# Kernel optimization log

Hardware: AMD Instinct MI355X
Metric: run time of the kernel (lower is better)

## Reference

```python
import jax, jax.numpy as jnp
import numpy as np

INPUT_SIZE = 128
HIDDEN_SIZE = 128
B, S = 4, 4096


def setup_inputs() -> dict:
    key = jax.random.key(0)
    ks = jax.random.split(key, 9)
    sc_in = 1.0 / np.sqrt(INPUT_SIZE)
    sc_h = 1.0 / np.sqrt(HIDDEN_SIZE)
    return {
        "x": jax.random.normal(ks[0], (B, S, INPUT_SIZE), jnp.float32),
        "Wq": jax.random.uniform(ks[1], (INPUT_SIZE, HIDDEN_SIZE), jnp.float32, -sc_in, sc_in),
        "bq": jax.random.uniform(ks[2], (HIDDEN_SIZE,), jnp.float32, -sc_in, sc_in),
        "Wk": jax.random.uniform(ks[3], (INPUT_SIZE, HIDDEN_SIZE), jnp.float32, -sc_in, sc_in),
        "bk": jax.random.uniform(ks[4], (HIDDEN_SIZE,), jnp.float32, -sc_in, sc_in),
        "Wv": jax.random.uniform(ks[5], (INPUT_SIZE, HIDDEN_SIZE), jnp.float32, -sc_in, sc_in),
        "bv": jax.random.uniform(ks[6], (HIDDEN_SIZE,), jnp.float32, -sc_in, sc_in),
        "Wo": jax.random.uniform(ks[7], (HIDDEN_SIZE, INPUT_SIZE), jnp.float32, -sc_h, sc_h),
        "bo": jax.random.uniform(ks[8], (INPUT_SIZE,), jnp.float32, -sc_h, sc_h),
    }


def reference(x, Wq, bq, Wk, bk, Wv, bv, Wo, bo):
    # single-head scaled dot-product attention (non-causal), dropout is eval-mode identity
    q = x @ Wq + bq                      # [B, S, H]
    k = x @ Wk + bk                      # [B, S, H]
    v = x @ Wv + bv                      # [B, S, H]
    scale = 1.0 / jnp.sqrt(jnp.asarray(HIDDEN_SIZE, x.dtype))
    scores = jnp.einsum("bsh,bth->bst", q, k) * scale   # [B, S, S]
    attn = jax.nn.softmax(scores, axis=-1)
    attended = jnp.einsum("bst,bth->bsh", attn, v)       # [B, S, H]
    return attended @ Wo + bo                            # [B, S, input_size]
```

## Files before the change

### kernel.cpp

```cpp
#include <hip/hip_runtime.h>
#include <stdint.h>

typedef __attribute__((ext_vector_type(8))) short short8;
typedef __attribute__((ext_vector_type(4))) float f32x4;
typedef __attribute__((ext_vector_type(16))) float f32x16;
typedef __attribute__((ext_vector_type(4))) int i32x4;
typedef __attribute__((ext_vector_type(2))) int i32x2;

#define MFMA16(a, b, c) __builtin_amdgcn_mfma_f32_16x16x32_bf16((a), (b), (c), 0, 0, 0)
#define MFMA32(a, b, c) __builtin_amdgcn_mfma_f32_32x32x16_bf16((a), (b), (c), 0, 0, 0)

typedef __attribute__((address_space(1))) const void GVoid;
typedef __attribute__((address_space(3))) void LVoid;
#define GLDS16(g, l) __builtin_amdgcn_global_load_lds((GVoid*)(g), (LVoid*)(l), 16, 0, 0)

#define L2E 1.4426950408889634f

__device__ __forceinline__ unsigned short f2bf(float f) {
  unsigned int u = __builtin_bit_cast(unsigned int, f);
  u += 0x7fffu + ((u >> 16) & 1u);
  return (unsigned short)(u >> 16);
}
__device__ __forceinline__ float bf2f(unsigned short u) {
  return __builtin_bit_cast(float, (unsigned int)u << 16);
}

__device__ __forceinline__ float fexp2(float x) {
  return __builtin_amdgcn_exp2f(x);
}

__device__ __forceinline__ i32x2 pls(int a, int b) {
  return __builtin_amdgcn_permlane32_swap(a, b, false, false);
}
__device__ __forceinline__ float fasf(int x) { return __builtin_bit_cast(float, x); }
__device__ __forceinline__ int iasi(float x) { return __builtin_bit_cast(int, x); }

__device__ __forceinline__ int cvtpk(float lo, float hi) {
  int d;
  asm("v_cvt_pk_bf16_f32 %0, %1, %2" : "=v"(d) : "v"(lo), "v"(hi));
  return d;
}

__global__ __launch_bounds__(256) void k_proj(
    const float* __restrict__ x,
    const float* __restrict__ Wq, const float* __restrict__ bq,
    const float* __restrict__ Wk, const float* __restrict__ bk,
    const float* __restrict__ Wv, const float* __restrict__ bv,
    const float* __restrict__ Wo,
    unsigned short* __restrict__ Q2, unsigned short* __restrict__ K2,
    unsigned short* __restrict__ V2, unsigned short* __restrict__ Wo2)
{
  __shared__ __align__(16) unsigned short wt[128 * 128];
  __shared__ __align__(16) unsigned short st[64 * 136];
  const int tid  = threadIdx.x;
  const int lane = tid & 63;
  const int wid  = tid >> 6;
  const int l15  = lane & 15;
  const int g    = lane >> 4;
  const int wI   = blockIdx.x >> 8;
  const int blk  = blockIdx.x & 255;
  const int r0   = blk * 64 + wid * 16;

  if (blockIdx.x == 0) {
    for (int e = tid; e < 16384; e += 256) {
      int j = e & 7, ln = (e >> 3) & 63, kt = (e >> 9) & 7, dt = e >> 12;
      int h = kt * 16 + (ln >> 5) * 8 + j, oc = dt * 32 + (ln & 31);
      Wo2[e] = f2bf(Wo[h * 128 + oc]);
    }
  }

  short8 af[4];
  {
    const float* xp = x + (r0 + l15) * 128 + g * 8;
#pragma unroll
    for (int kt = 0; kt < 4; ++kt) {
      float4 v0 = *(const float4*)(xp + kt * 32);
      float4 v1 = *(const float4*)(xp + kt * 32 + 4);
      short8 a;
      a[0] = (short)f2bf(v0.x); a[1] = (short)f2bf(v0.y);
      a[2] = (short)f2bf(v0.z); a[3] = (short)f2bf(v0.w);
      a[4] = (short)f2bf(v1.x); a[5] = (short)f2bf(v1.y);
      a[6] = (short)f2bf(v1.z); a[7] = (short)f2bf(v1.w);
      af[kt] = a;
    }
  }

  const float* W  = (wI == 0) ? Wq : (wI == 1) ? Wk : Wv;
  const float* bv_ = (wI == 0) ? bq : (wI == 1) ? bk : bv;

  for (int i = 0; i < 64; ++i) {
    int idx = i * 256 + tid;
    int k = idx >> 7, n = idx & 127;
    int cs = (k >> 3) ^ (n & 7);
    wt[n * 128 + cs * 8 + (k & 7)] = f2bf(W[idx]);
  }
  __syncthreads();

  float bias[8];
#pragma unroll
  for (int nt = 0; nt < 8; ++nt) bias[nt] = bv_[nt * 16 + l15];

  f32x4 acc[8];
#pragma unroll
  for (int nt = 0; nt < 8; ++nt) acc[nt] = (f32x4){0.f, 0.f, 0.f, 0.f};

#pragma unroll
  for (int nt = 0; nt < 8; ++nt) {
    const int n = nt * 16 + l15;
#pragma unroll
    for (int ks = 0; ks < 4; ++ks) {
      int cs = (ks * 4 + g) ^ (n & 7);
      short8 bf = *(const short8*)&wt[n * 128 + cs * 8];
      acc[nt] = MFMA16(af[ks], bf, acc[nt]);
    }
  }

  if (wI < 2) {
    const float sc = (wI == 0) ? 0.08838834764831845f : 1.0f;
#pragma unroll
    for (int nt = 0; nt < 8; ++nt) {
      int col = nt * 16 + l15;
#pragma unroll
      for (int r = 0; r < 4; ++r)
        st[(wid * 16 + g * 4 + r) * 136 + col] = f2bf((acc[nt][r] + bias[nt]) * sc);
    }
    __syncthreads();
    unsigned short* Og = (wI == 0) ? Q2 : K2;
#pragma unroll
    for (int c4 = 0; c4 < 4; ++c4) {
      int c = c4 * 256 + tid;
      int T = c >> 9, cc = c & 511;
      int kt = cc >> 6, hib = (cc >> 5) & 1, s32 = cc & 31;
      int m0 = blk * 64 + T * 32;
      int bb = m0 >> 12, tile = (m0 & 4095) >> 5;
      short8 v = *(const short8*)&st[(T * 32 + s32) * 136 + kt * 16 + hib * 8];
      *(short8*)&Og[(size_t)(bb * 128 + tile) * 4096 + cc * 8] = v;
    }
  } else {
#pragma unroll
    for (int nt = 0; nt < 8; ++nt) {
      int col = nt * 16 + l15;
      int m0 = r0 + g * 4;
      int bb = m0 >> 12, srow = m0 & 4095;
      int idx = (bb * 128 + (srow >> 5)) * 4096 + ((srow >> 4) & 1) * 2048 +
                (col >> 5) * 512 + ((srow >> 3) & 1) * 256 + (col & 31) * 8 +
                (srow & 7);
      ushort4 pk;
      pk.x = f2bf(acc[nt][0] + bias[nt]);
      pk.y = f2bf(acc[nt][1] + bias[nt]);
      pk.z = f2bf(acc[nt][2] + bias[nt]);
      pk.w = f2bf(acc[nt][3] + bias[nt]);
      *(ushort4*)&V2[idx] = pk;
    }
  }
}

__global__ __launch_bounds__(256, 2) void k_attn(
    const unsigned short* __restrict__ Q2,
    const unsigned short* __restrict__ K2,
    const unsigned short* __restrict__ V2,
    unsigned short* __restrict__ PA,
    float* __restrict__ MLl)
{
  __shared__ __align__(16) char smem[65536];
  const int tid = threadIdx.x, lane = tid & 63, wid = tid >> 6;
  const int rr = lane & 31, hi = lane >> 5;
  const int p = blockIdx.x;
  const int b = (p & 7) >> 1;
  const int idx = ((p >> 3) << 1) | (p & 1);
  const int qst = idx >> 2, kvq = idx & 3;
  const int q0tile = qst * 4 + wid;

  short8 qf[8];
  {
    const unsigned short* qp = Q2 + (size_t)(b * 128 + q0tile) * 4096 + lane * 8;
#pragma unroll
    for (int kt = 0; kt < 8; ++kt) qf[kt] = *(const short8*)(qp + kt * 512);
  }

  const unsigned short* gsrc[4];
  gsrc[0] = K2 + (size_t)(b * 128 + kvq * 32 + 0) * 4096 + tid * 8;
  gsrc[1] = K2 + (size_t)(b * 128 + kvq * 32 + 1) * 4096 + tid * 8;
  gsrc[2] = V2 + (size_t)(b * 128 + kvq * 32 + 0) * 4096 + tid * 8;
  gsrc[3] = V2 + (size_t)(b * 128 + kvq * 32 + 1) * 4096 + tid * 8;

#pragma unroll
  for (int i = 0; i < 4; ++i) {
    GLDS16(gsrc[i], smem + i * 8192 + tid * 16);
    GLDS16(gsrc[i] + 2048, smem + i * 8192 + 4096 + tid * 16);
  }

  f32x16 O[4];
#pragma unroll
  for (int dt = 0; dt < 4; ++dt)
#pragma unroll
    for (int j = 0; j < 16; ++j) O[dt][j] = 0.f;
  f32x16 zc;
#pragma unroll
  for (int j = 0; j < 16; ++j) zc[j] = 0.f;
  float lS = 0.f;

  for (int t = 0; t < 16; ++t) {
    char* const b0 = smem + (t & 1) * 32768;
    asm volatile("s_waitcnt vmcnt(0)" ::: "memory");
    __builtin_amdgcn_s_barrier();
    if (t < 15) {
      char* const bn = smem + ((t + 1) & 1) * 32768;
      const size_t adv = (size_t)(t + 1) * 8192;
#pragma unroll
      for (int i = 0; i < 4; ++i) {
        GLDS16(gsrc[i] + adv, bn + i * 8192 + tid * 16);
        GLDS16(gsrc[i] + adv + 2048, bn + i * 8192 + 4096 + tid * 16);
      }
    }
    __builtin_amdgcn_sched_barrier(0);

    f32x16 sT0, sT1;
    __builtin_amdgcn_s_setprio(1);
    {
      short8 kf[8];
#pragma unroll
      for (int kt = 0; kt < 8; ++kt)
        kf[kt] = *(const short8*)(b0 + kt * 1024 + lane * 16);
      sT0 = MFMA32(kf[0], qf[0], zc);
#pragma unroll
      for (int kt = 1; kt < 8; ++kt) sT0 = MFMA32(kf[kt], qf[kt], sT0);
    }
    {
      short8 kf[8];
#pragma unroll
      for (int kt = 0; kt < 8; ++kt)
        kf[kt] = *(const short8*)(b0 + 8192 + kt * 1024 + lane * 16);
      sT1 = MFMA32(kf[0], qf[0], zc);
#pragma unroll
      for (int kt = 1; kt < 8; ++kt) sT1 = MFMA32(kf[kt], qf[kt], sT1);
    }
    __builtin_amdgcn_s_setprio(0);

    {
      float pv[16];
#pragma unroll
      for (int r = 0; r < 16; ++r) pv[r] = fexp2(sT0[r] * L2E);
      float s01 = (pv[0] + pv[1]) + (pv[2] + pv[3]);
      float s23 = (pv[4] + pv[5]) + (pv[6] + pv[7]);
      float s45 = (pv[8] + pv[9]) + (pv[10] + pv[11]);
      float s67 = (pv[12] + pv[13]) + (pv[14] + pv[15]);
      float ts = (s01 + s23) + (s45 + s67);
      { i32x2 r = pls(iasi(ts), iasi(ts)); ts = fasf(r[0]) + fasf(r[1]); }
      lS += ts;

      short8 pa0, pa1;
      {
        int dw[8];
#pragma unroll
        for (int m = 0; m < 8; ++m) dw[m] = cvtpk(pv[2 * m], pv[2 * m + 1]);
        i32x2 ra = pls(dw[0], dw[2]);
        i32x2 rb = pls(dw[1], dw[3]);
        i32x2 rc = pls(dw[4], dw[6]);
        i32x2 rd = pls(dw[5], dw[7]);
        i32x4 w0 = {ra[0], rb[0], ra[1], rb[1]};
        i32x4 w1 = {rc[0], rd[0], rc[1], rd[1]};
        pa0 = __builtin_bit_cast(short8, w0);
        pa1 = __builtin_bit_cast(short8, w1);
      }

      __builtin_amdgcn_s_setprio(1);
      {
        const char* vb = b0 + 16384;
        short8 vf[4];
#pragma unroll
        for (int dt = 0; dt < 4; ++dt)
          vf[dt] = *(const short8*)(vb + dt * 1024 + lane * 16);
#pragma unroll
        for (int dt = 0; dt < 4; ++dt) O[dt] = MFMA32(pa0, vf[dt], O[dt]);
#pragma unroll
        for (int dt = 0; dt < 4; ++dt)
          vf[dt] = *(const short8*)(vb + 4096 + dt * 1024 + lane * 16);
#pragma unroll
        for (int dt = 0; dt < 4; ++dt) O[dt] = MFMA32(pa1, vf[dt], O[dt]);
      }
      __builtin_amdgcn_s_setprio(0);
    }

    {
      float pv[16];
#pragma unroll
      for (int r = 0; r < 16; ++r) pv[r] = fexp2(sT1[r] * L2E);
      float s01 = (pv[0] + pv[1]) + (pv[2] + pv[3]);
      float s23 = (pv[4] + pv[5]) + (pv[6] + pv[7]);
      float s45 = (pv[8] + pv[9]) + (pv[10] + pv[11]);
      float s67 = (pv[12] + pv[13]) + (pv[14] + pv[15]);
      float ts = (s01 + s23) + (s45 + s67);
      { i32x2 r = pls(iasi(ts), iasi(ts)); ts = fasf(r[0]) + fasf(r[1]); }
      lS += ts;

      short8 pa2, pa3;
      {
        int dw[8];
#pragma unroll
        for (int m = 0; m < 8; ++m) dw[m] = cvtpk(pv[2 * m], pv[2 * m + 1]);
        i32x2 ra = pls(dw[0], dw[2]);
        i32x2 rb = pls(dw[1], dw[3]);
        i32x2 rc = pls(dw[4], dw[6]);
        i32x2 rd = pls(dw[5], dw[7]);
        i32x4 w0 = {ra[0], rb[0], ra[1], rb[1]};
        i32x4 w1 = {rc[0], rd[0], rc[1], rd[1]};
        pa2 = __builtin_bit_cast(short8, w0);
        pa3 = __builtin_bit_cast(short8, w1);
      }

      __builtin_amdgcn_s_setprio(1);
      {
        const char* vb = b0 + 16384 + 8192;
        short8 vf[4];
#pragma unroll
        for (int dt = 0; dt < 4; ++dt)
          vf[dt] = *(const short8*)(vb + dt * 1024 + lane * 16);
#pragma unroll
        for (int dt = 0; dt < 4; ++dt) O[dt] = MFMA32(pa2, vf[dt], O[dt]);
#pragma unroll
        for (int dt = 0; dt < 4; ++dt)
          vf[dt] = *(const short8*)(vb + 4096 + dt * 1024 + lane * 16);
#pragma unroll
        for (int dt = 0; dt < 4; ++dt) O[dt] = MFMA32(pa3, vf[dt], O[dt]);
      }
      __builtin_amdgcn_s_setprio(0);
    }
  }

  unsigned short* pab = PA + ((size_t)(b * 4 + kvq) * 128 + q0tile) * 4096;
#pragma unroll
  for (int dt = 0; dt < 4; ++dt) {
    int kt = dt * 2 + (rr >> 4);
#pragma unroll
    for (int r = 0; r < 16; ++r) {
      int q = (r & 3) + 8 * (r >> 2) + 4 * hi;
      int e = kt * 512 + (((rr >> 3) & 1) * 32 + q) * 8 + (rr & 7);
      pab[e] = f2bf(O[dt][r]);
    }
  }
  if (hi == 0)
    MLl[(size_t)(b * 4 + kvq) * 4096 + q0tile * 32 + rr] = lS;
}

__global__ __launch_bounds__(256) void k_merge(
    const unsigned short* __restrict__ PA,
    const float* __restrict__ MLl,
    const unsigned short* __restrict__ Wo2,
    const float* __restrict__ bo,
    float* __restrict__ out)
{
  const int tid = threadIdx.x, lane = tid & 63, w = tid >> 6;
  const int rr = lane & 31, hi = lane >> 5;
  const int p = blockIdx.x;
  const int b = (p & 7) >> 1;
  const int qt32 = ((p >> 3) << 1) | (p & 1);

  float L = 0.f;
#pragma unroll
  for (int h = 0; h < 4; ++h)
    L += MLl[(size_t)(b * 4 + h) * 4096 + qt32 * 32 + rr];
  float iL = 1.0f / L;

  short8 attb[8];
#pragma unroll
  for (int kt = 0; kt < 8; ++kt) {
    float a[8];
#pragma unroll
    for (int j = 0; j < 8; ++j) a[j] = 0.f;
#pragma unroll
    for (int h = 0; h < 4; ++h) {
      short8 ph = *(const short8*)(PA + ((size_t)(b * 4 + h) * 128 + qt32) * 4096 +
                                   kt * 512 + lane * 8);
#pragma unroll
      for (int j = 0; j < 8; ++j)
        a[j] += bf2f((unsigned short)ph[j]);
    }
#pragma unroll
    for (int j = 0; j < 8; ++j) a[j] *= iL;
    i32x4 wv = {cvtpk(a[0], a[1]), cvtpk(a[2], a[3]),
                cvtpk(a[4], a[5]), cvtpk(a[6], a[7])};
    attb[kt] = __builtin_bit_cast(short8, wv);
  }

  short8 wof[8];
#pragma unroll
  for (int kt = 0; kt < 8; ++kt)
    wof[kt] = *(const short8*)(Wo2 + (w * 8 + kt) * 512 + lane * 8);

  f32x16 zc;
#pragma unroll
  for (int j = 0; j < 16; ++j) zc[j] = 0.f;
  f32x16 acc = MFMA32(attb[0], wof[0], zc);
#pragma unroll
  for (int kt = 1; kt < 8; ++kt) acc = MFMA32(attb[kt], wof[kt], acc);

  float bov = bo[w * 32 + rr];
  float* op = out + (size_t)(b * 4096 + qt32 * 32) * 128 + w * 32 + rr;
#pragma unroll
  for (int r = 0; r < 16; ++r) {
    int q = (r & 3) + 8 * (r >> 2) + 4 * hi;
    op[q * 128] = acc[r] + bov;
  }
}

extern "C" void kernel_launch(void* const* d_in, const int* in_sizes, int n_in,
                              void* d_out, int out_size, void* d_ws, size_t ws_size,
                              hipStream_t stream) {
  const float* x  = (const float*)d_in[0];
  const float* Wq = (const float*)d_in[1];
  const float* bq = (const float*)d_in[2];
  const float* Wk = (const float*)d_in[3];
  const float* bk = (const float*)d_in[4];
  const float* Wv = (const float*)d_in[5];
  const float* bv = (const float*)d_in[6];
  const float* Wo = (const float*)d_in[7];
  const float* bo = (const float*)d_in[8];

  const size_t NE = 4u * 4096u * 128u;
  unsigned short* Q2  = (unsigned short*)d_ws;
  unsigned short* K2  = Q2 + NE;
  unsigned short* V2  = K2 + NE;
  unsigned short* Wo2 = V2 + NE;
  unsigned short* PA  = Wo2 + 16384;
  float*          MLl = (float*)(PA + (size_t)16 * 128 * 4096);

  k_proj<<<768, 256, 0, stream>>>(x, Wq, bq, Wk, bk, Wv, bv, Wo, Q2, K2, V2, Wo2);
  k_attn<<<512, 256, 0, stream>>>(Q2, K2, V2, PA, MLl);
  k_merge<<<512, 256, 0, stream>>>(PA, MLl, Wo2, bo, (float*)d_out);
}
```

Measured before the change: 73.48 us.

## Store attention partials in MFMA accumulator order and permute through LDS in merge

The attention kernel now writes its partial output as contiguous 16-byte packed bf16 vectors in accumulator register order, replacing scattered 2-byte stores. The merge kernel takes over the layout permutation: each wave sums its slice of the four partials, scatters the fp32 sums into shared memory in the required fragment layout, syncs, then reads them back as MFMA operands. This trades uncoalesced global stores in the heavy kernel for an LDS round trip and a barrier in the light merge kernel. It also cuts redundant global reads in merge, since each wave previously reloaded all four partials.

New measurement: 70.54 us, median of 2. 4.0% less time.

```diff
diff --git a/kernel.cpp b/kernel.cpp
--- a/kernel.cpp
+++ b/kernel.cpp
@@ -164,7 +164,6 @@
 {
   __shared__ __align__(16) char smem[65536];
   const int tid = threadIdx.x, lane = tid & 63, wid = tid >> 6;
-  const int rr = lane & 31, hi = lane >> 5;
   const int p = blockIdx.x;
   const int b = (p & 7) >> 1;
   const int idx = ((p >> 3) << 1) | (p & 1);
@@ -330,17 +329,16 @@
 
   unsigned short* pab = PA + ((size_t)(b * 4 + kvq) * 128 + q0tile) * 4096;
 #pragma unroll
-  for (int dt = 0; dt < 4; ++dt) {
-    int kt = dt * 2 + (rr >> 4);
-#pragma unroll
-    for (int r = 0; r < 16; ++r) {
-      int q = (r & 3) + 8 * (r >> 2) + 4 * hi;
-      int e = kt * 512 + (((rr >> 3) & 1) * 32 + q) * 8 + (rr & 7);
-      pab[e] = f2bf(O[dt][r]);
-    }
-  }
-  if (hi == 0)
-    MLl[(size_t)(b * 4 + kvq) * 4096 + q0tile * 32 + rr] = lS;
+  for (int c = 0; c < 8; ++c) {
+    int dt = c >> 1, r0 = (c & 1) * 8;
+    i32x4 wv = {cvtpk(O[dt][r0 + 0], O[dt][r0 + 1]),
+                cvtpk(O[dt][r0 + 2], O[dt][r0 + 3]),
+                cvtpk(O[dt][r0 + 4], O[dt][r0 + 5]),
+                cvtpk(O[dt][r0 + 6], O[dt][r0 + 7])};
+    *(short8*)(pab + c * 512 + lane * 8) = __builtin_bit_cast(short8, wv);
+  }
+  if ((lane >> 5) == 0)
+    MLl[(size_t)(b * 4 + kvq) * 4096 + q0tile * 32 + (lane & 31)] = lS;
 }
 
 __global__ __launch_bounds__(256) void k_merge(
@@ -350,12 +348,47 @@
     const float* __restrict__ bo,
     float* __restrict__ out)
 {
+  __shared__ __align__(16) float att[8 * 64 * 8];
   const int tid = threadIdx.x, lane = tid & 63, w = tid >> 6;
   const int rr = lane & 31, hi = lane >> 5;
   const int p = blockIdx.x;
   const int b = (p & 7) >> 1;
   const int qt32 = ((p >> 3) << 1) | (p & 1);
 
+  const int pl = lane;
+  float a[2][8];
+#pragma unroll
+  for (int c2 = 0; c2 < 2; ++c2)
+#pragma unroll
+    for (int j = 0; j < 8; ++j) a[c2][j] = 0.f;
+#pragma unroll
+  for (int h = 0; h < 4; ++h) {
+    const unsigned short* pb = PA + ((size_t)(b * 4 + h) * 128 + qt32) * 4096;
+#pragma unroll
+    for (int c2 = 0; c2 < 2; ++c2) {
+      short8 ph = *(const short8*)(pb + (w * 2 + c2) * 512 + pl * 8);
+#pragma unroll
+      for (int j = 0; j < 8; ++j)
+        a[c2][j] += bf2f((unsigned short)ph[j]);
+    }
+  }
+
+#pragma unroll
+  for (int c2 = 0; c2 < 2; ++c2) {
+    int c = w * 2 + c2, dt = c >> 1;
+    int kt = dt * 2 + ((pl & 31) >> 4);
+    int shalf = ((pl & 31) >> 3) & 1;
+    int jd = pl & 7;
+#pragma unroll
+    for (int j = 0; j < 8; ++j) {
+      int r = (c & 1) * 8 + j;
+      int row = (r & 3) + 8 * (r >> 2) + 4 * (pl >> 5);
+      int s = shalf * 32 + row;
+      att[kt * 512 + s * 8 + jd] = a[c2][j];
+    }
+  }
+  __syncthreads();
+
   float L = 0.f;
 #pragma unroll
   for (int h = 0; h < 4; ++h)
@@ -365,21 +398,10 @@
   short8 attb[8];
 #pragma unroll
   for (int kt = 0; kt < 8; ++kt) {
-    float a[8];
-#pragma unroll
-    for (int j = 0; j < 8; ++j) a[j] = 0.f;
-#pragma unroll
-    for (int h = 0; h < 4; ++h) {
-      short8 ph = *(const short8*)(PA + ((size_t)(b * 4 + h) * 128 + qt32) * 4096 +
-                                   kt * 512 + lane * 8);
-#pragma unroll
-      for (int j = 0; j < 8; ++j)
-        a[j] += bf2f((unsigned short)ph[j]);
-    }
-#pragma unroll
-    for (int j = 0; j < 8; ++j) a[j] *= iL;
-    i32x4 wv = {cvtpk(a[0], a[1]), cvtpk(a[2], a[3]),
-                cvtpk(a[4], a[5]), cvtpk(a[6], a[7])};
+    f32x4 lo = *(const f32x4*)&att[kt * 512 + lane * 8];
+    f32x4 hi4 = *(const f32x4*)&att[kt * 512 + lane * 8 + 4];
+    i32x4 wv = {cvtpk(lo[0] * iL, lo[1] * iL), cvtpk(lo[2] * iL, lo[3] * iL),
+                cvtpk(hi4[0] * iL, hi4[1] * iL), cvtpk(hi4[2] * iL, hi4[3] * iL)};
     attb[kt] = __builtin_bit_cast(short8, wv);
   }
 
```
